# Kernel tuning notes

Measured on AMD Instinct MI355X. Metric: run time of the kernel, lower is better.

Reference implementation:

```python
import jax, jax.numpy as jnp
import numpy as np

NUM_GROUPS = 32
EPS = 1e-6


def setup_inputs() -> dict:
    key = jax.random.key(0)
    ks = jax.random.split(key, 8)
    B, H, W, C = 2, 64, 64, 512
    heads, hd = 8, 64
    s = 0.02
    return {
        "x": jax.random.normal(ks[0], (B, H, W, C), jnp.float32),
        "gn_scale": jnp.ones((C,), jnp.float32),
        "gn_bias": jnp.zeros((C,), jnp.float32),
        "wq": jax.random.normal(ks[1], (C, heads, hd), jnp.float32) * s,
        "bq": jnp.zeros((heads, hd), jnp.float32),
        "wk": jax.random.normal(ks[2], (C, heads, hd), jnp.float32) * s,
        "bk": jnp.zeros((heads, hd), jnp.float32),
        "wv": jax.random.normal(ks[3], (C, heads, hd), jnp.float32) * s,
        "bv": jnp.zeros((heads, hd), jnp.float32),
        "wo": jax.random.normal(ks[4], (heads, hd, C), jnp.float32) * s,
        "bo": jnp.zeros((C,), jnp.float32),
    }


def _group_norm(x, scale, bias):
    # flax GroupNorm defaults: 32 groups, eps=1e-6, reduce over spatial + within-group channels
    B, H, W, C = x.shape
    g = NUM_GROUPS
    xg = x.reshape(B, H, W, g, C // g)
    mean = jnp.mean(xg, axis=(1, 2, 4), keepdims=True)
    var = jnp.mean(jnp.square(xg - mean), axis=(1, 2, 4), keepdims=True)
    xn = (xg - mean) * jax.lax.rsqrt(var + EPS)
    return xn.reshape(B, H, W, C) * scale + bias


def reference(x, gn_scale, gn_bias, wq, bq, wk, bk, wv, bv, wo, bo):
    B, H, W, C = x.shape
    hd = wq.shape[-1]
    h = _group_norm(x.astype(jnp.float32), gn_scale, gn_bias).astype(x.dtype)
    h = h.reshape(B, H * W, C)  # [B, S, C]
    q = jnp.einsum("bsc,chd->bshd", h, wq) + bq
    k = jnp.einsum("bsc,chd->bshd", h, wk) + bk
    v = jnp.einsum("bsc,chd->bshd", h, wv) + bv
    # standard scaled dot-product attention (head-split in source is mathematically identical)
    logits = jnp.einsum("bqhd,bkhd->bhqk", q * (hd ** -0.5), k)  # [B, h, S, S]
    attn = jax.nn.softmax(logits, axis=-1)
    o = jnp.einsum("bhqk,bkhd->bqhd", attn, v).astype(jnp.float32)
    out = jnp.einsum("bshd,hdc->bsc", o, wo) + bo
    return x + out.reshape(B, H, W, C)
```

## Files before the change

### kernel.cpp

```cpp
#include <hip/hip_runtime.h>
#include <hip/hip_bf16.h>

typedef __attribute__((ext_vector_type(8))) short bf16x8;
typedef __attribute__((ext_vector_type(4))) float f32x4;
typedef __attribute__((ext_vector_type(16))) float f32x16;

#define MFMA16(a, b, c) __builtin_amdgcn_mfma_f32_16x16x32_bf16(a, b, c, 0, 0, 0)
#define MFMA32(a, b, c) __builtin_amdgcn_mfma_f32_32x32x16_bf16(a, b, c, 0, 0, 0)

static constexpr int Bn = 2;
static constexpr int S  = 4096;
static constexpr int C  = 512;
static constexpr int NH = 8;
static constexpr int HD = 64;
static constexpr int M  = Bn * S;

#define QSCALE 0.18033688f

__device__ __forceinline__ ushort f2bf(float f) {
  unsigned u = __builtin_bit_cast(unsigned, f);
  u += 0x7fffu + ((u >> 16) & 1u);
  return (ushort)(u >> 16);
}

__device__ __forceinline__ float bf2f(ushort u) {
  return __builtin_bit_cast(float, (unsigned)u << 16);
}

__device__ __forceinline__ unsigned pkbf(float a, float b) {
  return (unsigned)f2bf(a) | ((unsigned)f2bf(b) << 16);
}

__device__ __forceinline__ unsigned cvtpk(float a, float b) {
  unsigned r;
  asm("v_cvt_pk_bf16_f32 %0, %1, %2" : "=v"(r) : "v"(a), "v"(b));
  return r;
}

#define GLOAD_LDS16(g, l) __builtin_amdgcn_global_load_lds( \
    (const __attribute__((address_space(1))) unsigned*)(const void*)(g), \
    (__attribute__((address_space(3))) unsigned*)(void*)(l), 16, 0, 0)

__global__ __launch_bounds__(256) void prep_kernel(const float* __restrict__ x,
                                                   float2* __restrict__ stats,
                                                   const float* __restrict__ w0,
                                                   const float* __restrict__ w1,
                                                   const float* __restrict__ w2,
                                                   const float* __restrict__ w3,
                                                   ushort* __restrict__ wT) {
  __shared__ float tile[64][65];
  __shared__ float2 red[4];
  if (blockIdx.x < 64) {
    int bg = blockIdx.x;
    int b = bg >> 5, g = bg & 31;
    const float* xp = x + (size_t)b * S * C + g * 16;
    float sum = 0.f, sq = 0.f;
    for (int s = threadIdx.x; s < S; s += 256) {
      const float4* p = (const float4*)(xp + (size_t)s * C);
      #pragma unroll
      for (int i = 0; i < 4; i++) {
        float4 v = p[i];
        sum += v.x + v.y + v.z + v.w;
        sq  += v.x * v.x + v.y * v.y + v.z * v.z + v.w * v.w;
      }
    }
    #pragma unroll
    for (int d = 1; d < 64; d <<= 1) {
      sum += __shfl_xor(sum, d);
      sq  += __shfl_xor(sq, d);
    }
    if ((threadIdx.x & 63) == 0) red[threadIdx.x >> 6] = make_float2(sum, sq);
    __syncthreads();
    if (threadIdx.x == 0) {
      float s0 = 0.f, q0 = 0.f;
      #pragma unroll
      for (int i = 0; i < 4; i++) { s0 += red[i].x; q0 += red[i].y; }
      float inv = 1.f / (float)(S * 16);
      float mean = s0 * inv;
      float var = q0 * inv - mean * mean;
      stats[bg] = make_float2(mean, rsqrtf(var + 1e-6f));
    }
  } else {
    int bid = blockIdx.x - 64;
    int mat = bid >> 6;
    int xx = bid & 63;
    const float* w = (mat == 0) ? w0 : (mat == 1) ? w1 : (mat == 2) ? w2 : w3;
    int tr = (xx >> 3) * 64;
    int tc = (xx & 7) * 64;
    int ty = threadIdx.x >> 6, tx = threadIdx.x & 63;
    #pragma unroll
    for (int i = 0; i < 16; i++) {
      int r = i * 4 + ty;
      tile[r][tx] = w[(size_t)(tr + r) * 512 + tc + tx];
    }
    __syncthreads();
    #pragma unroll
    for (int i = 0; i < 16; i++) {
      int r = i * 4 + ty;
      wT[((size_t)mat << 18) + (size_t)(tc + r) * 512 + tr + tx] = f2bf(tile[tx][r]);
    }
  }
}

__global__ __launch_bounds__(256) void gn_apply_kernel(const float* __restrict__ x,
                                                       const float* __restrict__ sc,
                                                       const float* __restrict__ bi,
                                                       const float2* __restrict__ stats,
                                                       ushort* __restrict__ h) {
  int i = blockIdx.x * 256 + threadIdx.x;
  int s = i >> 6;
  int c0 = (i & 63) << 3;
  int b = s >> 12;
  float2 st = stats[(b << 5) + (c0 >> 4)];
  const float4* xv = (const float4*)(x + (size_t)s * C + c0);
  const float4* sv = (const float4*)(sc + c0);
  const float4* bv = (const float4*)(bi + c0);
  float4 a0 = xv[0], a1 = xv[1];
  float4 s0 = sv[0], s1 = sv[1];
  float4 b0 = bv[0], b1 = bv[1];
  uint4 pk;
  pk.x = pkbf((a0.x - st.x) * st.y * s0.x + b0.x, (a0.y - st.x) * st.y * s0.y + b0.y);
  pk.y = pkbf((a0.z - st.x) * st.y * s0.z + b0.z, (a0.w - st.x) * st.y * s0.w + b0.w);
  pk.z = pkbf((a1.x - st.x) * st.y * s1.x + b1.x, (a1.y - st.x) * st.y * s1.y + b1.y);
  pk.w = pkbf((a1.z - st.x) * st.y * s1.z + b1.z, (a1.w - st.x) * st.y * s1.w + b1.w);
  *(uint4*)(h + (size_t)i * 8) = pk;
}

__global__ __launch_bounds__(256, 3) void qkv_gemm_kernel(const ushort* __restrict__ h,
                                                          const ushort* __restrict__ wT,
                                                          const float* __restrict__ bq,
                                                          const float* __restrict__ bk,
                                                          const float* __restrict__ bv,
                                                          ushort* __restrict__ qo,
                                                          ushort* __restrict__ ko,
                                                          ushort* __restrict__ vT) {
  __shared__ ushort SM[4][4096];
  const int t = threadIdx.x;
  const int l = t & 63;
  const int w = t >> 6;
  const int lr = l & 15, lg = l >> 4;
  const int m0 = blockIdx.x * 128, n0 = blockIdx.y * 128;
  const int mw = (w >> 1) * 64, nw = (w & 1) * 64;

  const ushort* Ab = h  + (size_t)m0 * C;
  const ushort* Bb = wT + (size_t)n0 * C;

  {
    GLOAD_LDS16(Ab + (size_t)(t >> 2) * C + (t & 3) * 8,           &SM[0][t * 8]);
    GLOAD_LDS16(Ab + (size_t)(64 + (t >> 2)) * C + (t & 3) * 8,    &SM[0][(t + 256 - 512) * 8 + 4096]);
    GLOAD_LDS16(Bb + (size_t)(t >> 2) * C + (t & 3) * 8,           &SM[2][t * 8]);
    GLOAD_LDS16(Bb + (size_t)(64 + (t >> 2)) * C + (t & 3) * 8,    &SM[2][(t + 256 - 512) * 8 + 4096]);
  }
  __syncthreads();

  f32x4 acc[4][4] = {};
  int buf = 0;
  for (int kt = 0; kt < 16; kt++) {
    if (kt + 1 < 16) {
      int k0 = (kt + 1) * 32;
      int nb = buf ^ 1;
      GLOAD_LDS16(Ab + (size_t)(t >> 2) * C + k0 + (t & 3) * 8,        &SM[nb][t * 8]);
      GLOAD_LDS16(Ab + (size_t)(64 + (t >> 2)) * C + k0 + (t & 3) * 8, &SM[nb][(t + 256 - 512) * 8 + 4096]);
      GLOAD_LDS16(Bb + (size_t)(t >> 2) * C + k0 + (t & 3) * 8,        &SM[2 + nb][t * 8]);
      GLOAD_LDS16(Bb + (size_t)(64 + (t >> 2)) * C + k0 + (t & 3) * 8, &SM[2 + nb][(t + 256 - 512) * 8 + 4096]);
    }
    bf16x8 af[4], bfr[4];
    #pragma unroll
    for (int i = 0; i < 2; i++) af[i]      = *(const bf16x8*)&SM[buf][(mw + i * 16 + lr) * 32 + lg * 8];
    #pragma unroll
    for (int i = 2; i < 4; i++) af[i]      = *(const bf16x8*)&SM[buf][(mw + i * 16 + lr - 128) * 32 + lg * 8 + 4096];
    #pragma unroll
    for (int i = 0; i < 2; i++) bfr[i]     = *(const bf16x8*)&SM[2 + buf][(nw + i * 16 + lr) * 32 + lg * 8];
    #pragma unroll
    for (int i = 2; i < 4; i++) bfr[i]     = *(const bf16x8*)&SM[2 + buf][(nw + i * 16 + lr - 128) * 32 + lg * 8 + 4096];
    #pragma unroll
    for (int mi = 0; mi < 4; mi++)
      #pragma unroll
      for (int ni = 0; ni < 4; ni++)
        acc[mi][ni] = MFMA16(af[mi], bfr[ni], acc[mi][ni]);
    __syncthreads();
    buf ^= 1;
  }

  const int mat = n0 >> 9;
  const int cg0 = n0 & 511;
  if (mat == 2) {
    ushort* Tr = &SM[0][0];
    #pragma unroll
    for (int mi = 0; mi < 4; mi++) {
      #pragma unroll
      for (int ni = 0; ni < 4; ni++) {
        #pragma unroll
        for (int r = 0; r < 4; r++) {
          int s_loc = mw + mi * 16 + lg * 4 + r;
          int sp = (s_loc & ~12) | ((s_loc & 4) << 1) | ((s_loc & 8) >> 1);
          int c_loc = nw + ni * 16 + lr;
          Tr[c_loc * 128 + (sp ^ ((c_loc & 7) << 3))] = f2bf(acc[mi][ni][r] + bv[cg0 + c_loc]);
        }
      }
    }
    __syncthreads();
    const int c_loc = t >> 1, s2 = (t & 1) * 64;
    const size_t rowb = ((size_t)((m0 >> 12) * C + cg0 + c_loc)) * S + (m0 & (S - 1));
    #pragma unroll
    for (int j = 0; j < 8; j++) {
      int ch = (s2 + j * 8) ^ ((c_loc & 7) << 3);
      *(uint4*)(vT + rowb + s2 + j * 8) = *(const uint4*)&Tr[c_loc * 128 + ch];
    }
  } else {
    #pragma unroll
    for (int mi = 0; mi < 4; mi++) {
      #pragma unroll
      for (int ni = 0; ni < 4; ni++) {
        #pragma unroll
        for (int r = 0; r < 4; r++) {
          int srow = m0 + mw + mi * 16 + lg * 4 + r;
          int nl = cg0 + nw + ni * 16 + lr;
          float v = acc[mi][ni][r];
          if (mat == 0) {
            qo[(size_t)srow * C + nl] = f2bf((v + bq[nl]) * QSCALE);
          } else {
            ko[(size_t)srow * C + nl] = f2bf(v + bk[nl]);
          }
        }
      }
    }
  }
}

__global__ __launch_bounds__(512, 4) void attn_kernel(const ushort* __restrict__ q,
                                                      const ushort* __restrict__ k,
                                                      const ushort* __restrict__ vT,
                                                      ushort* __restrict__ o) {
  __shared__ ushort KtF[2][2][64 * 64];
  __shared__ ushort VtF[2][2][64 * 64];

  const int l = threadIdx.x & 63;
  const int wid = threadIdx.x >> 6;
  const int khalf = wid >> 2;
  const int wq = wid & 3;
  const int l31 = l & 31;
  const int hi = l >> 5;
  const int bh = blockIdx.y;
  const int b = bh >> 3, hh = bh & 7;
  const int q0 = blockIdx.x * 128 + wq * 32;
  const int k0 = khalf * (S / 2);
  constexpr int NT = (S / 2) / 64;

  const ushort* qp = q + ((size_t)(b * S + q0)) * C + hh * HD;
  const ushort* kp = k + ((size_t)(b * S + k0)) * C + hh * HD;
  const ushort* vp = vT + ((size_t)(b * C) + hh * HD) * S + k0;

  const int srow = wq * 16 + (l >> 3);
  const int sc   = l & 7;
  const int swz8 = (sc ^ (srow & 7)) * 8;
  const ushort* kpA = kp + (size_t)srow * C + swz8;
  const ushort* kpB = kpA + (size_t)8 * C;
  const ushort* vpA = vp + (size_t)srow * S + swz8;
  const ushort* vpB = vpA + (size_t)8 * S;
  const int ldsA = (wq * 2 + 0) * 512;
  const int ldsB = (wq * 2 + 1) * 512;
  ushort* Kg = &KtF[khalf][0][0];
  ushort* Vg = &VtF[khalf][0][0];

  bf16x8 qa[4];
  #pragma unroll
  for (int kd = 0; kd < 4; kd++)
    qa[kd] = *(const bf16x8*)(qp + (size_t)l31 * C + kd * 16 + hi * 8);

  f32x16 oacc[2] = {};
  float lst = 0.f;

#define ATTN_STAGE(BUF, T) { \
    GLOAD_LDS16(kpA + (size_t)(T) * (64 * C), Kg + (BUF) * 4096 + ldsA); \
    GLOAD_LDS16(kpB + (size_t)(T) * (64 * C), Kg + (BUF) * 4096 + ldsB); \
    GLOAD_LDS16(vpA + (T) * 64, Vg + (BUF) * 4096 + ldsA); \
    GLOAD_LDS16(vpB + (T) * 64, Vg + (BUF) * 4096 + ldsB); \
  }

#define ATTN_COMPUTE(BUF) \
  _Pragma("unroll") \
  for (int kn = 0; kn < 2; kn++) { \
    __builtin_amdgcn_s_setprio(1); \
    f32x16 s = {}; \
    _Pragma("unroll") \
    for (int kd = 0; kd < 4; kd++) { \
      bf16x8 kf = *(const bf16x8*)&Kg[(BUF) * 4096 + (kn * 32 + l31) * 64 + (((kd * 2 + hi) ^ (l31 & 7)) * 8)]; \
      s = MFMA32(kf, qa[kd], s); \
    } \
    __builtin_amdgcn_s_setprio(0); \
    float e[16]; \
    _Pragma("unroll") \
    for (int r = 0; r < 16; r++) e[r] = __builtin_amdgcn_exp2f(s[r]); \
    unsigned pw[8]; \
    _Pragma("unroll") \
    for (int j = 0; j < 8; j++) pw[j] = cvtpk(e[2 * j], e[2 * j + 1]); \
    lst += ((((e[0] + e[1]) + (e[2] + e[3])) + ((e[4] + e[5]) + (e[6] + e[7]))) \
          + (((e[8] + e[9]) + (e[10] + e[11])) + ((e[12] + e[13]) + (e[14] + e[15])))); \
    __builtin_amdgcn_s_setprio(1); \
    _Pragma("unroll") \
    for (int kc = 0; kc < 2; kc++) { \
      union { unsigned u[4]; bf16x8 v; } pu; \
      pu.u[0] = pw[kc * 4 + 0]; pu.u[1] = pw[kc * 4 + 1]; \
      pu.u[2] = pw[kc * 4 + 2]; pu.u[3] = pw[kc * 4 + 3]; \
      _Pragma("unroll") \
      for (int nd = 0; nd < 2; nd++) { \
        bf16x8 vf = *(const bf16x8*)&Vg[(BUF) * 4096 + (nd * 32 + l31) * 64 + ((((kn * 2 + kc) * 2 + hi) ^ (l31 & 7)) * 8)]; \
        oacc[nd] = MFMA32(pu.v, vf, oacc[nd]); \
      } \
    } \
    __builtin_amdgcn_s_setprio(0); \
  }

  ATTN_STAGE(0, 0);
  __syncthreads();

  for (int t2 = 0; t2 < NT; t2 += 2) {
    if (t2 + 1 < NT) ATTN_STAGE(1, t2 + 1);
    ATTN_COMPUTE(0);
    __syncthreads();
    if (t2 + 2 < NT) ATTN_STAGE(0, t2 + 2);
    ATTN_COMPUTE(1);
    __syncthreads();
  }

#undef ATTN_STAGE
#undef ATTN_COMPUTE

  ushort* Xo = &KtF[0][0][0];
  float*  Xl = (float*)&VtF[0][0][0];
  float lfull = lst + __shfl_xor(lst, 32);

  if (khalf == 1) {
    if (hi == 0) Xl[wq * 32 + l31] = lfull;
    #pragma unroll
    for (int r = 0; r < 16; r++) {
      int row = (r & 3) + 8 * (r >> 2) + 4 * hi;
      Xo[(wq * 32 + row) * 64 + l31]      = f2bf(oacc[0][r]);
      Xo[(wq * 32 + row) * 64 + 32 + l31] = f2bf(oacc[1][r]);
    }
  }
  __syncthreads();
  if (khalf == 0) {
    float ltot = lfull + Xl[wq * 32 + l31];
    #pragma unroll
    for (int r = 0; r < 16; r++) {
      int row = (r & 3) + 8 * (r >> 2) + 4 * hi;
      float inv = 1.0f / __shfl(ltot, row);
      float o0 = oacc[0][r] + bf2f(Xo[(wq * 32 + row) * 64 + l31]);
      float o1 = oacc[1][r] + bf2f(Xo[(wq * 32 + row) * 64 + 32 + l31]);
      size_t base = ((size_t)(b * S + q0 + row)) * C + hh * HD;
      o[base + l31]      = f2bf(o0 * inv);
      o[base + 32 + l31] = f2bf(o1 * inv);
    }
  }
}

__global__ __launch_bounds__(256, 3) void oproj_gemm_kernel(const ushort* __restrict__ o,
                                                            const ushort* __restrict__ woT,
                                                            const float* __restrict__ x,
                                                            const float* __restrict__ bo,
                                                            float* __restrict__ out) {
  __shared__ ushort As[2][128 * 32];
  __shared__ ushort Bs[2][128 * 32];
  const int t = threadIdx.x;
  const int l = t & 63;
  const int w = t >> 6;
  const int lr = l & 15, lg = l >> 4;
  const int m0 = blockIdx.x * 128, n0 = blockIdx.y * 128;
  const int mw = (w >> 1) * 64, nw = (w & 1) * 64;

  const ushort* Ab = o   + (size_t)m0 * C;
  const ushort* Bb = woT + (size_t)n0 * C;

  {
    GLOAD_LDS16(Ab + (size_t)(t >> 2) * C + (t & 3) * 8,           &As[0][t * 8]);
    GLOAD_LDS16(Ab + (size_t)(64 + (t >> 2)) * C + (t & 3) * 8,    &As[0][(t + 256) * 8]);
    GLOAD_LDS16(Bb + (size_t)(t >> 2) * C + (t & 3) * 8,           &Bs[0][t * 8]);
    GLOAD_LDS16(Bb + (size_t)(64 + (t >> 2)) * C + (t & 3) * 8,    &Bs[0][(t + 256) * 8]);
  }
  __syncthreads();

  f32x4 acc[4][4] = {};
  int buf = 0;
  for (int kt = 0; kt < 16; kt++) {
    if (kt + 1 < 16) {
      int k0 = (kt + 1) * 32;
      GLOAD_LDS16(Ab + (size_t)(t >> 2) * C + k0 + (t & 3) * 8,        &As[buf ^ 1][t * 8]);
      GLOAD_LDS16(Ab + (size_t)(64 + (t >> 2)) * C + k0 + (t & 3) * 8, &As[buf ^ 1][(t + 256) * 8]);
      GLOAD_LDS16(Bb + (size_t)(t >> 2) * C + k0 + (t & 3) * 8,        &Bs[buf ^ 1][t * 8]);
      GLOAD_LDS16(Bb + (size_t)(64 + (t >> 2)) * C + k0 + (t & 3) * 8, &Bs[buf ^ 1][(t + 256) * 8]);
    }
    bf16x8 af[4], bfr[4];
    #pragma unroll
    for (int i = 0; i < 4; i++) af[i]  = *(const bf16x8*)&As[buf][(mw + i * 16 + lr) * 32 + lg * 8];
    #pragma unroll
    for (int i = 0; i < 4; i++) bfr[i] = *(const bf16x8*)&Bs[buf][(nw + i * 16 + lr) * 32 + lg * 8];
    #pragma unroll
    for (int mi = 0; mi < 4; mi++)
      #pragma unroll
      for (int ni = 0; ni < 4; ni++)
        acc[mi][ni] = MFMA16(af[mi], bfr[ni], acc[mi][ni]);
    __syncthreads();
    buf ^= 1;
  }

  #pragma unroll
  for (int mi = 0; mi < 4; mi++) {
    #pragma unroll
    for (int ni = 0; ni < 4; ni++) {
      #pragma unroll
      for (int r = 0; r < 4; r++) {
        int srow = m0 + mw + mi * 16 + lg * 4 + r;
        int c = n0 + nw + ni * 16 + lr;
        out[(size_t)srow * C + c] = x[(size_t)srow * C + c] + acc[mi][ni][r] + bo[c];
      }
    }
  }
}

extern "C" void kernel_launch(void* const* d_in, const int* in_sizes, int n_in,
                              void* d_out, int out_size, void* d_ws, size_t ws_size,
                              hipStream_t stream) {
  const float* x  = (const float*)d_in[0];
  const float* gs = (const float*)d_in[1];
  const float* gb = (const float*)d_in[2];
  const float* wq = (const float*)d_in[3];
  const float* bq = (const float*)d_in[4];
  const float* wk = (const float*)d_in[5];
  const float* bk = (const float*)d_in[6];
  const float* wv = (const float*)d_in[7];
  const float* bv = (const float*)d_in[8];
  const float* wo = (const float*)d_in[9];
  const float* bo = (const float*)d_in[10];

  char* ws = (char*)d_ws;
  ushort* h    = (ushort*)(ws);
  ushort* wT   = (ushort*)(ws + 8388608);
  ushort* qb   = (ushort*)(ws + 10485760);
  ushort* kb   = (ushort*)(ws + 18874368);
  ushort* vTb  = (ushort*)(ws + 27262976);
  float2* st   = (float2*)(ws + 44040192);
  ushort* ofin = qb;

  prep_kernel<<<320, 256, 0, stream>>>(x, st, wq, wk, wv, wo, wT);
  gn_apply_kernel<<<2048, 256, 0, stream>>>(x, gs, gb, st, h);
  qkv_gemm_kernel<<<dim3(64, 12), 256, 0, stream>>>(h, wT, bq, bk, bv, qb, kb, vTb);
  attn_kernel<<<dim3(32, 16), 512, 0, stream>>>(qb, kb, vTb, ofin);
  oproj_gemm_kernel<<<dim3(64, 4), 256, 0, stream>>>(ofin, wT + 786432, x, bo, (float*)d_out);
}
```

Measured before the change: 150.2 us.

## Keep two global-to-LDS loads in flight with partial vmcnt waits

Restructures the QKV GEMM, attention and output-projection main loops so two tiles are prefetched ahead. Each loop now uses a raw s_barrier plus an explicit partial s_waitcnt vmcnt(4) instead of __syncthreads, which would wait for every outstanding load. The aim is to hide global load latency behind MFMA work and avoid draining the memory queue at each barrier. The risk is correctness: the partial wait count must match the number of loads issued per stage, and scheduling barriers limit how freely the compiler can reorder instructions.

```diff
diff --git a/kernel.cpp b/kernel.cpp
--- a/kernel.cpp
+++ b/kernel.cpp
@@ -16,6 +16,11 @@
 static constexpr int M  = Bn * S;
 
 #define QSCALE 0.18033688f
+
+#define VM_WAIT(N) do { asm volatile("s_waitcnt vmcnt(" #N ")" ::: "memory"); \
+                        __builtin_amdgcn_sched_barrier(0); } while (0)
+#define RAW_BAR() do { __builtin_amdgcn_sched_barrier(0); __builtin_amdgcn_s_barrier(); \
+                       __builtin_amdgcn_sched_barrier(0); } while (0)
 
 __device__ __forceinline__ ushort f2bf(float f) {
   unsigned u = __builtin_bit_cast(unsigned, f);
@@ -145,42 +150,44 @@
   const ushort* Ab = h  + (size_t)m0 * C;
   const ushort* Bb = wT + (size_t)n0 * C;
 
-  {
-    GLOAD_LDS16(Ab + (size_t)(t >> 2) * C + (t & 3) * 8,           &SM[0][t * 8]);
-    GLOAD_LDS16(Ab + (size_t)(64 + (t >> 2)) * C + (t & 3) * 8,    &SM[0][(t + 256 - 512) * 8 + 4096]);
-    GLOAD_LDS16(Bb + (size_t)(t >> 2) * C + (t & 3) * 8,           &SM[2][t * 8]);
-    GLOAD_LDS16(Bb + (size_t)(64 + (t >> 2)) * C + (t & 3) * 8,    &SM[2][(t + 256 - 512) * 8 + 4096]);
-  }
-  __syncthreads();
-
   f32x4 acc[4][4] = {};
-  int buf = 0;
-  for (int kt = 0; kt < 16; kt++) {
-    if (kt + 1 < 16) {
-      int k0 = (kt + 1) * 32;
-      int nb = buf ^ 1;
-      GLOAD_LDS16(Ab + (size_t)(t >> 2) * C + k0 + (t & 3) * 8,        &SM[nb][t * 8]);
-      GLOAD_LDS16(Ab + (size_t)(64 + (t >> 2)) * C + k0 + (t & 3) * 8, &SM[nb][(t + 256 - 512) * 8 + 4096]);
-      GLOAD_LDS16(Bb + (size_t)(t >> 2) * C + k0 + (t & 3) * 8,        &SM[2 + nb][t * 8]);
-      GLOAD_LDS16(Bb + (size_t)(64 + (t >> 2)) * C + k0 + (t & 3) * 8, &SM[2 + nb][(t + 256 - 512) * 8 + 4096]);
-    }
-    bf16x8 af[4], bfr[4];
-    #pragma unroll
-    for (int i = 0; i < 2; i++) af[i]      = *(const bf16x8*)&SM[buf][(mw + i * 16 + lr) * 32 + lg * 8];
-    #pragma unroll
-    for (int i = 2; i < 4; i++) af[i]      = *(const bf16x8*)&SM[buf][(mw + i * 16 + lr - 128) * 32 + lg * 8 + 4096];
-    #pragma unroll
-    for (int i = 0; i < 2; i++) bfr[i]     = *(const bf16x8*)&SM[2 + buf][(nw + i * 16 + lr) * 32 + lg * 8];
-    #pragma unroll
-    for (int i = 2; i < 4; i++) bfr[i]     = *(const bf16x8*)&SM[2 + buf][(nw + i * 16 + lr - 128) * 32 + lg * 8 + 4096];
-    #pragma unroll
-    for (int mi = 0; mi < 4; mi++)
-      #pragma unroll
-      for (int ni = 0; ni < 4; ni++)
-        acc[mi][ni] = MFMA16(af[mi], bfr[ni], acc[mi][ni]);
-    __syncthreads();
-    buf ^= 1;
-  }
+
+#define QKV_STAGE(BUF, KT) { \
+    int kk0 = (KT) * 32; \
+    GLOAD_LDS16(Ab + (size_t)(t >> 2) * C + kk0 + (t & 3) * 8,        &SM[BUF][t * 8]); \
+    GLOAD_LDS16(Ab + (size_t)(64 + (t >> 2)) * C + kk0 + (t & 3) * 8, &SM[BUF][t * 8 + 2048]); \
+    GLOAD_LDS16(Bb + (size_t)(t >> 2) * C + kk0 + (t & 3) * 8,        &SM[2 + (BUF)][t * 8]); \
+    GLOAD_LDS16(Bb + (size_t)(64 + (t >> 2)) * C + kk0 + (t & 3) * 8, &SM[2 + (BUF)][t * 8 + 2048]); \
+  }
+
+#define QKV_COMPUTE(BUF) { \
+    bf16x8 af[4], bfr[4]; \
+    _Pragma("unroll") \
+    for (int i = 0; i < 4; i++) af[i]  = *(const bf16x8*)&SM[BUF][(mw + i * 16 + lr) * 32 + lg * 8]; \
+    _Pragma("unroll") \
+    for (int i = 0; i < 4; i++) bfr[i] = *(const bf16x8*)&SM[2 + (BUF)][(nw + i * 16 + lr) * 32 + lg * 8]; \
+    _Pragma("unroll") \
+    for (int mi = 0; mi < 4; mi++) \
+      _Pragma("unroll") \
+      for (int ni = 0; ni < 4; ni++) \
+        acc[mi][ni] = MFMA16(af[mi], bfr[ni], acc[mi][ni]); \
+  }
+
+  QKV_STAGE(0, 0);
+  QKV_STAGE(1, 1);
+  VM_WAIT(4);
+  RAW_BAR();
+  for (int kt = 0; kt < 16; kt += 2) {
+    QKV_COMPUTE(0);
+    RAW_BAR();
+    if (kt + 2 < 16) { QKV_STAGE(0, kt + 2); VM_WAIT(4); } else { VM_WAIT(0); }
+    QKV_COMPUTE(1);
+    RAW_BAR();
+    if (kt + 3 < 16) { QKV_STAGE(1, kt + 3); VM_WAIT(4); } else { VM_WAIT(0); }
+  }
+
+#undef QKV_STAGE
+#undef QKV_COMPUTE
 
   const int mat = n0 >> 9;
   const int cg0 = n0 & 511;
@@ -313,19 +320,23 @@
   }
 
   ATTN_STAGE(0, 0);
-  __syncthreads();
+  ATTN_STAGE(1, 1);
+  VM_WAIT(4);
+  RAW_BAR();
 
   for (int t2 = 0; t2 < NT; t2 += 2) {
-    if (t2 + 1 < NT) ATTN_STAGE(1, t2 + 1);
     ATTN_COMPUTE(0);
-    __syncthreads();
-    if (t2 + 2 < NT) ATTN_STAGE(0, t2 + 2);
+    RAW_BAR();
+    if (t2 + 2 < NT) { ATTN_STAGE(0, t2 + 2); VM_WAIT(4); } else { VM_WAIT(0); }
     ATTN_COMPUTE(1);
-    __syncthreads();
+    RAW_BAR();
+    if (t2 + 3 < NT) { ATTN_STAGE(1, t2 + 3); VM_WAIT(4); } else { VM_WAIT(0); }
   }
 
 #undef ATTN_STAGE
 #undef ATTN_COMPUTE
+
+  __syncthreads();
 
   ushort* Xo = &KtF[0][0][0];
   float*  Xl = (float*)&VtF[0][0][0];
@@ -361,8 +372,8 @@
                                                             const float* __restrict__ x,
                                                             const float* __restrict__ bo,
                                                             float* __restrict__ out) {
-  __shared__ ushort As[2][128 * 32];
-  __shared__ ushort Bs[2][128 * 32];
+  __shared__ ushort As[2][4096];
+  __shared__ ushort Bs[2][4096];
   const int t = threadIdx.x;
   const int l = t & 63;
   const int w = t >> 6;
@@ -373,37 +384,44 @@
   const ushort* Ab = o   + (size_t)m0 * C;
   const ushort* Bb = woT + (size_t)n0 * C;
 
-  {
-    GLOAD_LDS16(Ab + (size_t)(t >> 2) * C + (t & 3) * 8,           &As[0][t * 8]);
-    GLOAD_LDS16(Ab + (size_t)(64 + (t >> 2)) * C + (t & 3) * 8,    &As[0][(t + 256) * 8]);
-    GLOAD_LDS16(Bb + (size_t)(t >> 2) * C + (t & 3) * 8,           &Bs[0][t * 8]);
-    GLOAD_LDS16(Bb + (size_t)(64 + (t >> 2)) * C + (t & 3) * 8,    &Bs[0][(t + 256) * 8]);
-  }
-  __syncthreads();
-
   f32x4 acc[4][4] = {};
-  int buf = 0;
-  for (int kt = 0; kt < 16; kt++) {
-    if (kt + 1 < 16) {
-      int k0 = (kt + 1) * 32;
-      GLOAD_LDS16(Ab + (size_t)(t >> 2) * C + k0 + (t & 3) * 8,        &As[buf ^ 1][t * 8]);
-      GLOAD_LDS16(Ab + (size_t)(64 + (t >> 2)) * C + k0 + (t & 3) * 8, &As[buf ^ 1][(t + 256) * 8]);
-      GLOAD_LDS16(Bb + (size_t)(t >> 2) * C + k0 + (t & 3) * 8,        &Bs[buf ^ 1][t * 8]);
-      GLOAD_LDS16(Bb + (size_t)(64 + (t >> 2)) * C + k0 + (t & 3) * 8, &Bs[buf ^ 1][(t + 256) * 8]);
-    }
-    bf16x8 af[4], bfr[4];
-    #pragma unroll
-    for (int i = 0; i < 4; i++) af[i]  = *(const bf16x8*)&As[buf][(mw + i * 16 + lr) * 32 + lg * 8];
-    #pragma unroll
-    for (int i = 0; i < 4; i++) bfr[i] = *(const bf16x8*)&Bs[buf][(nw + i * 16 + lr) * 32 + lg * 8];
-    #pragma unroll
-    for (int mi = 0; mi < 4; mi++)
-      #pragma unroll
-      for (int ni = 0; ni < 4; ni++)
-        acc[mi][ni] = MFMA16(af[mi], bfr[ni], acc[mi][ni]);
-    __syncthreads();
-    buf ^= 1;
-  }
+
+#define OP_STAGE(BUF, KT) { \
+    int kk0 = (KT) * 32; \
+    GLOAD_LDS16(Ab + (size_t)(t >> 2) * C + kk0 + (t & 3) * 8,        &As[BUF][t * 8]); \
+    GLOAD_LDS16(Ab + (size_t)(64 + (t >> 2)) * C + kk0 + (t & 3) * 8, &As[BUF][t * 8 + 2048]); \
+    GLOAD_LDS16(Bb + (size_t)(t >> 2) * C + kk0 + (t & 3) * 8,        &Bs[BUF][t * 8]); \
+    GLOAD_LDS16(Bb + (size_t)(64 + (t >> 2)) * C + kk0 + (t & 3) * 8, &Bs[BUF][t * 8 + 2048]); \
+  }
+
+#define OP_COMPUTE(BUF) { \
+    bf16x8 af[4], bfr[4]; \
+    _Pragma("unroll") \
+    for (int i = 0; i < 4; i++) af[i]  = *(const bf16x8*)&As[BUF][(mw + i * 16 + lr) * 32 + lg * 8]; \
+    _Pragma("unroll") \
+    for (int i = 0; i < 4; i++) bfr[i] = *(const bf16x8*)&Bs[BUF][(nw + i * 16 + lr) * 32 + lg * 8]; \
+    _Pragma("unroll") \
+    for (int mi = 0; mi < 4; mi++) \
+      _Pragma("unroll") \
+      for (int ni = 0; ni < 4; ni++) \
+        acc[mi][ni] = MFMA16(af[mi], bfr[ni], acc[mi][ni]); \
+  }
+
+  OP_STAGE(0, 0);
+  OP_STAGE(1, 1);
+  VM_WAIT(4);
+  RAW_BAR();
+  for (int kt = 0; kt < 16; kt += 2) {
+    OP_COMPUTE(0);
+    RAW_BAR();
+    if (kt + 2 < 16) { OP_STAGE(0, kt + 2); VM_WAIT(4); } else { VM_WAIT(0); }
+    OP_COMPUTE(1);
+    RAW_BAR();
+    if (kt + 3 < 16) { OP_STAGE(1, kt + 3); VM_WAIT(4); } else { VM_WAIT(0); }
+  }
+
+#undef OP_STAGE
+#undef OP_COMPUTE
 
   #pragma unroll
   for (int mi = 0; mi < 4; mi++) {
```

Measured after the change: 181.6 us. +21.0%, slower.

## Split group-norm statistics reduction across more blocks with partial sums

Applied to the files above, without the earlier changes.

The group-norm statistics pass previously used one block per (batch, group), so only 64 blocks each looped over all 4096 positions. It now launches 16 blocks per group, each reducing 256 positions into a partial sum and sum-of-squares. The apply kernel sums the 16 partials itself before normalising. This spreads the reduction over many more CUs. In exchange every apply thread reads 16 extra float2 values and repeats the finalisation math.

```diff
diff --git a/kernel.cpp b/kernel.cpp
--- a/kernel.cpp
+++ b/kernel.cpp
@@ -42,7 +42,7 @@
     (__attribute__((address_space(3))) unsigned*)(void*)(l), 16, 0, 0)
 
 __global__ __launch_bounds__(256) void prep_kernel(const float* __restrict__ x,
-                                                   float2* __restrict__ stats,
+                                                   float2* __restrict__ pstat,
                                                    const float* __restrict__ w0,
                                                    const float* __restrict__ w1,
                                                    const float* __restrict__ w2,
@@ -50,19 +50,18 @@
                                                    ushort* __restrict__ wT) {
   __shared__ float tile[64][65];
   __shared__ float2 red[4];
-  if (blockIdx.x < 64) {
-    int bg = blockIdx.x;
+  if (blockIdx.x < 1024) {
+    int bg = blockIdx.x >> 4;
+    int seg = blockIdx.x & 15;
     int b = bg >> 5, g = bg & 31;
-    const float* xp = x + (size_t)b * S * C + g * 16;
+    int s = seg * 256 + threadIdx.x;
+    const float4* p = (const float4*)(x + (size_t)b * S * C + (size_t)s * C + g * 16);
     float sum = 0.f, sq = 0.f;
-    for (int s = threadIdx.x; s < S; s += 256) {
-      const float4* p = (const float4*)(xp + (size_t)s * C);
-      #pragma unroll
-      for (int i = 0; i < 4; i++) {
-        float4 v = p[i];
-        sum += v.x + v.y + v.z + v.w;
-        sq  += v.x * v.x + v.y * v.y + v.z * v.z + v.w * v.w;
-      }
+    #pragma unroll
+    for (int i = 0; i < 4; i++) {
+      float4 v = p[i];
+      sum += v.x + v.y + v.z + v.w;
+      sq  += v.x * v.x + v.y * v.y + v.z * v.z + v.w * v.w;
     }
     #pragma unroll
     for (int d = 1; d < 64; d <<= 1) {
@@ -75,13 +74,10 @@
       float s0 = 0.f, q0 = 0.f;
       #pragma unroll
       for (int i = 0; i < 4; i++) { s0 += red[i].x; q0 += red[i].y; }
-      float inv = 1.f / (float)(S * 16);
-      float mean = s0 * inv;
-      float var = q0 * inv - mean * mean;
-      stats[bg] = make_float2(mean, rsqrtf(var + 1e-6f));
+      pstat[blockIdx.x] = make_float2(s0, q0);
     }
   } else {
-    int bid = blockIdx.x - 64;
+    int bid = blockIdx.x - 1024;
     int mat = bid >> 6;
     int xx = bid & 63;
     const float* w = (mat == 0) ? w0 : (mat == 1) ? w1 : (mat == 2) ? w2 : w3;
@@ -105,22 +101,30 @@
 __global__ __launch_bounds__(256) void gn_apply_kernel(const float* __restrict__ x,
                                                        const float* __restrict__ sc,
                                                        const float* __restrict__ bi,
-                                                       const float2* __restrict__ stats,
+                                                       const float2* __restrict__ pstat,
                                                        ushort* __restrict__ h) {
   int i = blockIdx.x * 256 + threadIdx.x;
   int s = i >> 6;
   int c0 = (i & 63) << 3;
   int b = s >> 12;
-  float2 st = stats[(b << 5) + (c0 >> 4)];
+  const float2* pp = &pstat[((b << 5) + (c0 >> 4)) * 16];
+  float s0 = 0.f, q0 = 0.f;
+  #pragma unroll
+  for (int j = 0; j < 16; j++) { float2 t = pp[j]; s0 += t.x; q0 += t.y; }
+  float invn = 1.f / (float)(S * 16);
+  float mean = s0 * invn;
+  float rsig = rsqrtf(q0 * invn - mean * mean + 1e-6f);
+  float2 st = make_float2(mean, rsig);
+
   const float4* xv = (const float4*)(x + (size_t)s * C + c0);
   const float4* sv = (const float4*)(sc + c0);
   const float4* bv = (const float4*)(bi + c0);
   float4 a0 = xv[0], a1 = xv[1];
-  float4 s0 = sv[0], s1 = sv[1];
+  float4 s0v = sv[0], s1 = sv[1];
   float4 b0 = bv[0], b1 = bv[1];
   uint4 pk;
-  pk.x = pkbf((a0.x - st.x) * st.y * s0.x + b0.x, (a0.y - st.x) * st.y * s0.y + b0.y);
-  pk.y = pkbf((a0.z - st.x) * st.y * s0.z + b0.z, (a0.w - st.x) * st.y * s0.w + b0.w);
+  pk.x = pkbf((a0.x - st.x) * st.y * s0v.x + b0.x, (a0.y - st.x) * st.y * s0v.y + b0.y);
+  pk.y = pkbf((a0.z - st.x) * st.y * s0v.z + b0.z, (a0.w - st.x) * st.y * s0v.w + b0.w);
   pk.z = pkbf((a1.x - st.x) * st.y * s1.x + b1.x, (a1.y - st.x) * st.y * s1.y + b1.y);
   pk.w = pkbf((a1.z - st.x) * st.y * s1.z + b1.z, (a1.w - st.x) * st.y * s1.w + b1.w);
   *(uint4*)(h + (size_t)i * 8) = pk;
@@ -440,11 +444,11 @@
   ushort* qb   = (ushort*)(ws + 10485760);
   ushort* kb   = (ushort*)(ws + 18874368);
   ushort* vTb  = (ushort*)(ws + 27262976);
-  float2* st   = (float2*)(ws + 44040192);
+  float2* pst  = (float2*)(ws + 44040192);
   ushort* ofin = qb;
 
-  prep_kernel<<<320, 256, 0, stream>>>(x, st, wq, wk, wv, wo, wT);
-  gn_apply_kernel<<<2048, 256, 0, stream>>>(x, gs, gb, st, h);
+  prep_kernel<<<1280, 256, 0, stream>>>(x, pst, wq, wk, wv, wo, wT);
+  gn_apply_kernel<<<2048, 256, 0, stream>>>(x, gs, gb, pst, h);
   qkv_gemm_kernel<<<dim3(64, 12), 256, 0, stream>>>(h, wT, bq, bk, bv, qb, kb, vTb);
   attn_kernel<<<dim3(32, 16), 512, 0, stream>>>(qb, kb, vTb, ofin);
   oproj_gemm_kernel<<<dim3(64, 4), 256, 0, stream>>>(ofin, wT + 786432, x, bo, (float*)d_out);
```

After: 143.7 us. 4.3% less time.
